# Performance work log

Hardware: AMD Instinct MI355X
Metric: run time of the kernel (lower is better)

Reference implementation:

```python
import jax, jax.numpy as jnp
import numpy as np

B, C, H, W = 8, 128, 48, 48
RED = 16  # SELayer reduction


def setup_inputs() -> dict:
    key = jax.random.key(0)
    ks = jax.random.split(key, 8)
    s = 0.05  # weight scale for numerical stability of softmax
    return {
        "x": jax.random.normal(ks[0], (B, C, H, W), jnp.float32),
        "Wq": jax.random.normal(ks[1], (C, C), jnp.float32) * s,
        "bq": jnp.zeros((C,), jnp.float32),
        "Wk": jax.random.normal(ks[2], (C, C), jnp.float32) * s,
        "bk": jnp.zeros((C,), jnp.float32),
        "Wv": jax.random.normal(ks[3], (C, C), jnp.float32) * s,
        "bv": jnp.zeros((C,), jnp.float32),
        "se_w1": jax.random.normal(ks[4], (C // RED, C), jnp.float32) * s,
        "se_w2": jax.random.normal(ks[5], (C, C // RED), jnp.float32) * s,
        "gamma": jax.random.normal(ks[6], (1,), jnp.float32),
    }


def reference(x, Wq, bq, Wk, bk, Wv, bv, se_w1, se_w2, gamma):
    b, c, h, w = x.shape
    n = h * w
    xf = x.reshape(b, c, n)  # (B, C, N)
    # 1x1 convs == per-pixel linear maps over channels
    q = jnp.einsum('oc,bcn->bon', Wq, xf) + bq[None, :, None]  # (B, C, N)
    k = jnp.einsum('oc,bcn->bon', Wk, xf) + bk[None, :, None]
    v = jnp.einsum('oc,bcn->bon', Wv, xf) + bv[None, :, None]
    # energy[b, i, j] = sum_c q[b, c, i] * k[b, c, j]  (unscaled, as in source)
    energy = jnp.einsum('bci,bcj->bij', q, k)  # (B, N, N)
    attn = jax.nn.softmax(energy, axis=-1)
    # out[b, c, i] = sum_j v[b, c, j] * attn[b, i, j]
    out = jnp.einsum('bcj,bij->bci', v, attn).reshape(b, c, h, w)
    # SELayer applied to the input x
    y = jnp.mean(x, axis=(2, 3))  # (B, C) global average pool
    y = jax.nn.relu(y @ se_w1.T)  # (B, C//RED)
    y = jax.nn.sigmoid(y @ se_w2.T)  # (B, C)
    x_se = x * y[:, :, None, None]
    return gamma[0] * out + x_se
```

## Files before the change

### kernel.cpp

```cpp
#include <hip/hip_runtime.h>

typedef _Float16 half8 __attribute__((ext_vector_type(8)));
typedef _Float16 half4 __attribute__((ext_vector_type(4)));
typedef _Float16 half2v __attribute__((ext_vector_type(2)));
typedef float f32x4 __attribute__((ext_vector_type(4)));

#define BATCH 8
#define CH 128
#define NPIX 2304
#define SPLIT 6
#define JPER (NPIX / SPLIT)
#define NT (JPER / 64)
#define BN (BATCH * NPIX)
#define LOG2E 1.44269504088896f

__device__ __forceinline__ f32x4 mfma32(half8 a, half8 b, f32x4 c) {
    return __builtin_amdgcn_mfma_f32_16x16x32_f16(a, b, c, 0, 0, 0);
}
__device__ __forceinline__ f32x4 mfma16(half4 a, half4 b, f32x4 c) {
    return __builtin_amdgcn_mfma_f32_16x16x16f16(a, b, c, 0, 0, 0);
}

__device__ __forceinline__ void gl_lds16(const _Float16* g, _Float16* l) {
    typedef const __attribute__((address_space(1))) unsigned int gu32;
    typedef __attribute__((address_space(3))) unsigned int lu32;
    __builtin_amdgcn_global_load_lds((gu32*)g, (lu32*)l, 16, 0, 0);
}

__global__ __launch_bounds__(256) void k_prep(
        const float* __restrict__ x, const float* __restrict__ Wq,
        const float* __restrict__ Wk, const float* __restrict__ Wv,
        _Float16* __restrict__ Wh, float* __restrict__ y0) {
    const int bid = blockIdx.x;
    const int t = threadIdx.x;
    if (bid < 1024) {
        const int row = bid;
        const float4* p = (const float4*)(x + (size_t)row * NPIX);
        float s = 0.f;
        for (int tt = t; tt < NPIX / 4; tt += 256) {
            float4 v = p[tt];
            s += v.x + v.y + v.z + v.w;
        }
        for (int m = 1; m < 64; m <<= 1) s += __shfl_xor(s, m);
        __shared__ float ls[4];
        if ((t & 63) == 0) ls[t >> 6] = s;
        __syncthreads();
        if (t == 0) y0[row] = (ls[0] + ls[1] + ls[2] + ls[3]) * (1.0f / (float)NPIX);
    } else {
        int i = (bid - 1024) * 256 + t;
        const float* src = (i < 16384) ? Wq : ((i < 32768) ? Wk : Wv);
        Wh[i] = (_Float16)src[i & 16383];
    }
}

__global__ __launch_bounds__(256) void k_proj(
        const float* __restrict__ x, const _Float16* __restrict__ Wh,
        const float* __restrict__ bq, const float* __restrict__ bk, const float* __restrict__ bv,
        _Float16* __restrict__ qT, _Float16* __restrict__ kT, _Float16* __restrict__ vN,
        const float* __restrict__ y0, const float* __restrict__ se_w1,
        const float* __restrict__ se_w2, float* __restrict__ scale) {
    const int which = blockIdx.z;
    const int t = threadIdx.x;

    if (which == 3) {
        if (blockIdx.x != 0 || blockIdx.y != 0) return;
        __shared__ float ly[128];
        __shared__ float ly1[8];
        for (int b = 0; b < BATCH; ++b) {
            if (t < 128) ly[t] = y0[b * 128 + t];
            __syncthreads();
            if (t < 8) {
                float a = 0.f;
                for (int c = 0; c < 128; ++c) a += se_w1[t * 128 + c] * ly[c];
                ly1[t] = fmaxf(a, 0.f);
            }
            __syncthreads();
            if (t < 128) {
                float a = 0.f;
                for (int r = 0; r < 8; ++r) a += se_w2[t * 8 + r] * ly1[r];
                scale[b * 128 + t] = 1.f / (1.f + __expf(-a));
            }
            __syncthreads();
        }
        return;
    }

    const int n0 = blockIdx.x * 128;
    const int b = blockIdx.y;
    const float* bias = (which == 0) ? bq : ((which == 1) ? bk : bv);
    const _Float16* W = Wh + which * 16384;

    __shared__ __align__(16) _Float16 xt[128 * 128];

    {
        const float* xb = x + (size_t)b * CH * NPIX + n0;
        for (int rep = 0; rep < 8; ++rep) {
            int flat = rep * 256 + t;
            int c2 = (flat >> 5) * 2;
            int n4 = (flat & 31) * 4;
            float4 va = *(const float4*)(xb + (size_t)c2 * NPIX + n4);
            float4 vb = *(const float4*)(xb + (size_t)(c2 + 1) * NPIX + n4);
            int cc = c2 & 7, ck = c2 >> 3;
            *(half2v*)(xt + (n4 + 0) * 128 + ((ck ^ ((n4 + 0) & 7)) * 8) + cc) =
                (half2v){(_Float16)va.x, (_Float16)vb.x};
            *(half2v*)(xt + (n4 + 1) * 128 + ((ck ^ ((n4 + 1) & 7)) * 8) + cc) =
                (half2v){(_Float16)va.y, (_Float16)vb.y};
            *(half2v*)(xt + (n4 + 2) * 128 + ((ck ^ ((n4 + 2) & 7)) * 8) + cc) =
                (half2v){(_Float16)va.z, (_Float16)vb.z};
            *(half2v*)(xt + (n4 + 3) * 128 + ((ck ^ ((n4 + 3) & 7)) * 8) + cc) =
                (half2v){(_Float16)va.w, (_Float16)vb.w};
        }
    }
    __syncthreads();

    const int lane = t & 63, w = t >> 6;
    const int ln15 = lane & 15, quad = lane >> 4;

    f32x4 zero4 = {0.f, 0.f, 0.f, 0.f};
    f32x4 acc[8][2];
    for (int mt = 0; mt < 8; ++mt) { acc[mt][0] = zero4; acc[mt][1] = zero4; }

    for (int ks = 0; ks < 4; ++ks) {
        half8 bf[2];
        for (int nt = 0; nt < 2; ++nt) {
            int row = w * 32 + nt * 16 + ln15;
            int ch = ks * 4 + quad;
            bf[nt] = *(const half8*)(xt + row * 128 + ((ch ^ (row & 7)) * 8));
        }
        for (int mt = 0; mt < 8; ++mt) {
            half8 af = *(const half8*)(W + (mt * 16 + ln15) * 128 + ks * 32 + quad * 8);
            acc[mt][0] = mfma32(af, bf[0], acc[mt][0]);
            acc[mt][1] = mfma32(af, bf[1], acc[mt][1]);
        }
    }
    __syncthreads();

    if (which == 2) {
        for (int mt = 0; mt < 8; ++mt)
            for (int nt = 0; nt < 2; ++nt)
                for (int r = 0; r < 4; ++r) {
                    int c = mt * 16 + quad * 4 + r;
                    int nl = w * 32 + nt * 16 + ln15;
                    xt[c * 128 + (((nl >> 3) ^ (c & 7)) * 8) + (nl & 7)] =
                        (_Float16)(acc[mt][nt][r] + bias[c]);
                }
        __syncthreads();
        _Float16* vb = vN + (size_t)b * CH * NPIX + n0;
        for (int rep = 0; rep < 8; ++rep) {
            int c = rep * 16 + (t >> 4), ch = t & 15;
            *(half8*)(vb + (size_t)c * NPIX + ch * 8) =
                *(const half8*)(xt + c * 128 + ((ch ^ (c & 7)) * 8));
        }
    } else {
        for (int mt = 0; mt < 8; ++mt)
            for (int nt = 0; nt < 2; ++nt)
                for (int r = 0; r < 4; r += 2) {
                    int c = mt * 16 + quad * 4 + r;
                    int nl = w * 32 + nt * 16 + ln15;
                    *(half2v*)(xt + nl * 128 + (((c >> 3) ^ (nl & 7)) * 8) + (c & 7)) =
                        (half2v){(_Float16)(acc[mt][nt][r] + bias[c]),
                                 (_Float16)(acc[mt][nt][r + 1] + bias[c + 1])};
                }
        __syncthreads();
        _Float16* dst = ((which == 0) ? qT : kT) + ((size_t)b * NPIX + n0) * CH;
        for (int rep = 0; rep < 8; ++rep) {
            int nl = rep * 16 + (t >> 4), ch = t & 15;
            *(half8*)(dst + nl * 128 + ch * 8) =
                *(const half8*)(xt + nl * 128 + ((ch ^ (nl & 7)) * 8));
        }
    }
}

__global__ __launch_bounds__(256, 5) void k_attn(
        const _Float16* __restrict__ qT, const _Float16* __restrict__ kT,
        const _Float16* __restrict__ vN,
        _Float16* __restrict__ o_part, float* __restrict__ g_m, float* __restrict__ g_l) {
    const int i0 = blockIdx.x * 64;
    const int b = blockIdx.y;
    const int split = blockIdx.z;
    const int t = threadIdx.x;
    const int lane = t & 63, w = t >> 6;
    const int ln15 = lane & 15, quad = lane >> 4;

    __shared__ __align__(16) _Float16 sh[16384];
    _Float16* k_s = sh;
    _Float16* v_s = sh + 8192;

    half8 qf[4];
    {
        const _Float16* qb = qT + ((size_t)b * NPIX + i0 + w * 16 + ln15) * CH + quad * 8;
        for (int kc = 0; kc < 4; ++kc) qf[kc] = *(const half8*)(qb + kc * 32);
    }

    const _Float16* kbase[4];
    const _Float16* vbase[4];
    #pragma unroll
    for (int r = 0; r < 4; ++r) {
        int idx = r * 4 + w;
        int row = 4 * idx + (lane >> 4);
        int kch = (lane & 15) ^ (row & 7);
        kbase[r] = kT + (size_t)b * NPIX * CH + (size_t)row * CH + kch * 8;
        int c = 8 * idx + (lane >> 3);
        int vch = (lane & 7) ^ (c & 7);
        vbase[r] = vN + (size_t)b * CH * NPIX + (size_t)c * NPIX + vch * 8;
    }

    auto stage = [&](int j0) {
        #pragma unroll
        for (int r = 0; r < 4; ++r)
            gl_lds16(kbase[r] + (size_t)j0 * CH, k_s + (r * 4 + w) * 512);
        #pragma unroll
        for (int r = 0; r < 4; ++r)
            gl_lds16(vbase[r] + j0, v_s + (r * 4 + w) * 512);
    };

    stage(split * JPER);

    f32x4 zero4 = {0.f, 0.f, 0.f, 0.f};
    f32x4 os[8];
    for (int ct = 0; ct < 8; ++ct) os[ct] = zero4;
    float m = -1e30f, l = 0.f;

    for (int it = 0; it < NT; ++it) {
        __syncthreads();

        f32x4 s[4];
        for (int jt = 0; jt < 4; ++jt) s[jt] = zero4;
        __builtin_amdgcn_s_setprio(1);
        for (int jt = 0; jt < 4; ++jt) {
            for (int kc = 0; kc < 4; ++kc) {
                int row = jt * 16 + ln15, ch = kc * 4 + quad;
                half8 kf = *(const half8*)(k_s + row * 128 + ((ch ^ (row & 7)) * 8));
                s[jt] = mfma32(kf, qf[kc], s[jt]);
            }
        }
        __builtin_amdgcn_s_setprio(0);

        float mx = fmaxf(fmaxf(s[0][0], s[0][1]), fmaxf(s[0][2], s[0][3]));
        for (int jt = 1; jt < 4; ++jt)
            mx = fmaxf(mx, fmaxf(fmaxf(s[jt][0], s[jt][1]), fmaxf(s[jt][2], s[jt][3])));
        mx = fmaxf(mx, __shfl_xor(mx, 16));
        mx = fmaxf(mx, __shfl_xor(mx, 32));
        if (!__all(mx - m <= 8.0f)) {
            float mnew = fmaxf(m, mx);
            float alpha = exp2f((m - mnew) * LOG2E);
            for (int ct = 0; ct < 8; ++ct) {
                os[ct][0] *= alpha; os[ct][1] *= alpha;
                os[ct][2] *= alpha; os[ct][3] *= alpha;
            }
            l *= alpha;
            m = mnew;
        }
        float mbias = m * LOG2E;

        float sum = 0.f;
        half4 pf[4];
        for (int jt = 0; jt < 4; ++jt)
            for (int r = 0; r < 4; ++r) {
                float p = exp2f(fmaf(s[jt][r], LOG2E, -mbias));
                sum += p;
                pf[jt][r] = (_Float16)p;
            }
        sum += __shfl_xor(sum, 16);
        sum += __shfl_xor(sum, 32);
        l += sum;

        __builtin_amdgcn_s_setprio(1);
        for (int ct = 0; ct < 8; ++ct) {
            int c = ct * 16 + ln15;
            for (int jt = 0; jt < 4; ++jt) {
                int chunk = jt * 2 + (quad >> 1);
                half4 vf = *(const half4*)(v_s + c * 64 + ((chunk ^ (c & 7)) * 8) + (quad & 1) * 4);
                os[ct] = mfma16(vf, pf[jt], os[ct]);
            }
        }
        __builtin_amdgcn_s_setprio(0);

        if (it < NT - 1) {
            __syncthreads();
            stage(split * JPER + (it + 1) * 64);
        }
    }

    if (quad == 0) {
        int i = i0 + w * 16 + ln15;
        g_m[(size_t)(split * BATCH + b) * NPIX + i] = m;
        g_l[(size_t)(split * BATCH + b) * NPIX + i] = l;
    }
    const float linv = 1.0f / l;
    __syncthreads();
    for (int ct = 0; ct < 8; ++ct)
        for (int r = 0; r < 4; ++r) {
            int c = ct * 16 + quad * 4 + r;
            int il = w * 16 + ln15;
            int chunk = (il >> 3);
            sh[c * 64 + ((chunk ^ (c & 7)) * 8) + (il & 7)] = (_Float16)(os[ct][r] * linv);
        }
    __syncthreads();
    _Float16* op = o_part + (size_t)(split * BATCH + b) * CH * NPIX;
    for (int rep = 0; rep < 4; ++rep) {
        int c = rep * 32 + (t >> 3), ch = t & 7;
        *(half8*)(op + (size_t)c * NPIX + i0 + ch * 8) =
            *(const half8*)(sh + c * 64 + ((ch ^ (c & 7)) * 8));
    }
}

__global__ __launch_bounds__(256) void k_combine(
        const _Float16* __restrict__ o_part, const float* __restrict__ g_m,
        const float* __restrict__ g_l, const float* __restrict__ x,
        const float* __restrict__ scale, const float* __restrict__ gamma_p,
        float* __restrict__ out) {
    const int i0 = blockIdx.x * 64;
    const int b = blockIdx.y;
    const int t = threadIdx.x;
    __shared__ float wl[SPLIT][64];

    if (t < 64) {
        int i = i0 + t;
        float mm[SPLIT], llv[SPLIT];
        float M = -1e30f;
        for (int s = 0; s < SPLIT; ++s) {
            mm[s] = g_m[(size_t)(s * BATCH + b) * NPIX + i];
            llv[s] = g_l[(size_t)(s * BATCH + b) * NPIX + i];
            M = fmaxf(M, mm[s]);
        }
        float L = 0.f, e[SPLIT];
        for (int s = 0; s < SPLIT; ++s) {
            e[s] = exp2f((mm[s] - M) * LOG2E);
            L += e[s] * llv[s];
        }
        float inv = 1.f / L;
        for (int s = 0; s < SPLIT; ++s) wl[s][t] = e[s] * llv[s] * inv;
    }
    __syncthreads();

    const float g = gamma_p[0];
    for (int rep = 0; rep < 4; ++rep) {
        int c = rep * 32 + (t >> 3), i8 = (t & 7) * 8;
        size_t base = ((size_t)b * CH + c) * NPIX + i0 + i8;
        float acc[8] = {0.f, 0.f, 0.f, 0.f, 0.f, 0.f, 0.f, 0.f};
        for (int s = 0; s < SPLIT; ++s) {
            half8 o = *(const half8*)(o_part +
                ((size_t)(s * BATCH + b) * CH + c) * NPIX + i0 + i8);
            for (int e = 0; e < 8; ++e) acc[e] += wl[s][i8 + e] * (float)o[e];
        }
        float sc = scale[b * 128 + c];
        float4 x0 = *(const float4*)(x + base);
        float4 x1 = *(const float4*)(x + base + 4);
        float4 r0, r1;
        r0.x = g * acc[0] + x0.x * sc; r0.y = g * acc[1] + x0.y * sc;
        r0.z = g * acc[2] + x0.z * sc; r0.w = g * acc[3] + x0.w * sc;
        r1.x = g * acc[4] + x1.x * sc; r1.y = g * acc[5] + x1.y * sc;
        r1.z = g * acc[6] + x1.z * sc; r1.w = g * acc[7] + x1.w * sc;
        *(float4*)(out + base) = r0;
        *(float4*)(out + base + 4) = r1;
    }
}

extern "C" void kernel_launch(void* const* d_in, const int* in_sizes, int n_in,
                              void* d_out, int out_size, void* d_ws, size_t ws_size,
                              hipStream_t stream) {
    const float* x     = (const float*)d_in[0];
    const float* Wq    = (const float*)d_in[1];
    const float* bq    = (const float*)d_in[2];
    const float* Wk    = (const float*)d_in[3];
    const float* bk    = (const float*)d_in[4];
    const float* Wv    = (const float*)d_in[5];
    const float* bv    = (const float*)d_in[6];
    const float* se_w1 = (const float*)d_in[7];
    const float* se_w2 = (const float*)d_in[8];
    const float* gamma = (const float*)d_in[9];
    float* out = (float*)d_out;

    char* ws = (char*)d_ws;
    const size_t E = (size_t)BATCH * NPIX * CH;
    _Float16* qT = (_Float16*)(ws);
    _Float16* kT = (_Float16*)(ws + E * 2);
    _Float16* vN = (_Float16*)(ws + E * 4);
    _Float16* op = (_Float16*)(ws + E * 6);
    char* tail   = ws + E * 6 + (size_t)SPLIT * E * 2;
    _Float16* Wh = (_Float16*)(tail);
    float* g_m   = (float*)(tail + 98304);
    float* g_l   = (float*)(tail + 98304 + (size_t)SPLIT * BN * 4);
    float* y0    = (float*)(tail + 98304 + 2 * (size_t)SPLIT * BN * 4);
    float* scale = (float*)(tail + 98304 + 2 * (size_t)SPLIT * BN * 4 + 4096);

    k_prep<<<1216, 256, 0, stream>>>(x, Wq, Wk, Wv, Wh, y0);
    k_proj<<<dim3(NPIX / 128, BATCH, 4), 256, 0, stream>>>(
        x, Wh, bq, bk, bv, qT, kT, vN, y0, se_w1, se_w2, scale);
    k_attn<<<dim3(NPIX / 64, BATCH, SPLIT), 256, 0, stream>>>(
        qT, kT, vN, op, g_m, g_l);
    k_combine<<<dim3(NPIX / 64, BATCH), 256, 0, stream>>>(
        op, g_m, g_l, x, scale, gamma, out);
}
```

Before: 167.8 us.

## Process 128 query rows per attention block to reuse K/V tiles across two halves

Each wave in the attention kernel now handles two 16-row query groups, so every K and V fragment read from LDS feeds two MFMAs. This halves K/V staging traffic per query row. The async global-to-LDS loads are replaced by synchronous register-staged copies with two barriers per tile. The lazy rescale skip and priority hints are dropped, and partial outputs are now stored unnormalised, with the combine step changed to match. The risks are more register pressure (launch bounds drop to 2 blocks per CU), fewer blocks, and loads no longer overlapping compute.

```diff
diff --git a/kernel.cpp b/kernel.cpp
--- a/kernel.cpp
+++ b/kernel.cpp
@@ -19,12 +19,6 @@
 }
 __device__ __forceinline__ f32x4 mfma16(half4 a, half4 b, f32x4 c) {
     return __builtin_amdgcn_mfma_f32_16x16x16f16(a, b, c, 0, 0, 0);
-}
-
-__device__ __forceinline__ void gl_lds16(const _Float16* g, _Float16* l) {
-    typedef const __attribute__((address_space(1))) unsigned int gu32;
-    typedef __attribute__((address_space(3))) unsigned int lu32;
-    __builtin_amdgcn_global_load_lds((gu32*)g, (lu32*)l, 16, 0, 0);
 }
 
 __global__ __launch_bounds__(256) void k_prep(
@@ -171,11 +165,11 @@
     }
 }
 
-__global__ __launch_bounds__(256, 5) void k_attn(
+__global__ __launch_bounds__(256, 2) void k_attn(
         const _Float16* __restrict__ qT, const _Float16* __restrict__ kT,
         const _Float16* __restrict__ vN,
         _Float16* __restrict__ o_part, float* __restrict__ g_m, float* __restrict__ g_l) {
-    const int i0 = blockIdx.x * 64;
+    const int i0 = blockIdx.x * 128;
     const int b = blockIdx.y;
     const int split = blockIdx.z;
     const int t = threadIdx.x;
@@ -186,122 +180,130 @@
     _Float16* k_s = sh;
     _Float16* v_s = sh + 8192;
 
-    half8 qf[4];
-    {
-        const _Float16* qb = qT + ((size_t)b * NPIX + i0 + w * 16 + ln15) * CH + quad * 8;
-        for (int kc = 0; kc < 4; ++kc) qf[kc] = *(const half8*)(qb + kc * 32);
-    }
-
-    const _Float16* kbase[4];
-    const _Float16* vbase[4];
+    half8 qf[2][4];
     #pragma unroll
-    for (int r = 0; r < 4; ++r) {
-        int idx = r * 4 + w;
-        int row = 4 * idx + (lane >> 4);
-        int kch = (lane & 15) ^ (row & 7);
-        kbase[r] = kT + (size_t)b * NPIX * CH + (size_t)row * CH + kch * 8;
-        int c = 8 * idx + (lane >> 3);
-        int vch = (lane & 7) ^ (c & 7);
-        vbase[r] = vN + (size_t)b * CH * NPIX + (size_t)c * NPIX + vch * 8;
-    }
-
-    auto stage = [&](int j0) {
-        #pragma unroll
-        for (int r = 0; r < 4; ++r)
-            gl_lds16(kbase[r] + (size_t)j0 * CH, k_s + (r * 4 + w) * 512);
-        #pragma unroll
-        for (int r = 0; r < 4; ++r)
-            gl_lds16(vbase[r] + j0, v_s + (r * 4 + w) * 512);
-    };
-
-    stage(split * JPER);
+    for (int ih = 0; ih < 2; ++ih) {
+        const _Float16* qb = qT + ((size_t)b * NPIX + i0 + w * 32 + ih * 16 + ln15) * CH + quad * 8;
+        #pragma unroll
+        for (int kc = 0; kc < 4; ++kc) qf[ih][kc] = *(const half8*)(qb + kc * 32);
+    }
 
     f32x4 zero4 = {0.f, 0.f, 0.f, 0.f};
-    f32x4 os[8];
-    for (int ct = 0; ct < 8; ++ct) os[ct] = zero4;
-    float m = -1e30f, l = 0.f;
+    f32x4 os[2][8];
+    #pragma unroll
+    for (int ih = 0; ih < 2; ++ih)
+        for (int ct = 0; ct < 8; ++ct) os[ih][ct] = zero4;
+    float m[2] = {-1e30f, -1e30f}, l[2] = {0.f, 0.f};
 
     for (int it = 0; it < NT; ++it) {
-        __syncthreads();
-
-        f32x4 s[4];
-        for (int jt = 0; jt < 4; ++jt) s[jt] = zero4;
-        __builtin_amdgcn_s_setprio(1);
+        const int j0 = split * JPER + it * 64;
+        __syncthreads();
+        {
+            const _Float16* kb = kT + ((size_t)b * NPIX + j0) * CH;
+            for (int rep = 0; rep < 4; ++rep) {
+                int row = rep * 16 + (t >> 4), ch = t & 15;
+                *(half8*)(k_s + row * 128 + ((ch ^ (row & 7)) * 8)) =
+                    *(const half8*)(kb + row * CH + ch * 8);
+            }
+        }
+        {
+            const _Float16* vb = vN + (size_t)b * CH * NPIX + j0;
+            for (int rep = 0; rep < 4; ++rep) {
+                int c = rep * 32 + (t >> 3), ch = t & 7;
+                *(half8*)(v_s + c * 64 + ((ch ^ (c & 7)) * 8)) =
+                    *(const half8*)(vb + (size_t)c * NPIX + ch * 8);
+            }
+        }
+        __syncthreads();
+
+        f32x4 s[2][4];
+        #pragma unroll
+        for (int jt = 0; jt < 4; ++jt) { s[0][jt] = zero4; s[1][jt] = zero4; }
+        #pragma unroll
         for (int jt = 0; jt < 4; ++jt) {
+            #pragma unroll
             for (int kc = 0; kc < 4; ++kc) {
                 int row = jt * 16 + ln15, ch = kc * 4 + quad;
                 half8 kf = *(const half8*)(k_s + row * 128 + ((ch ^ (row & 7)) * 8));
-                s[jt] = mfma32(kf, qf[kc], s[jt]);
-            }
-        }
-        __builtin_amdgcn_s_setprio(0);
-
-        float mx = fmaxf(fmaxf(s[0][0], s[0][1]), fmaxf(s[0][2], s[0][3]));
-        for (int jt = 1; jt < 4; ++jt)
-            mx = fmaxf(mx, fmaxf(fmaxf(s[jt][0], s[jt][1]), fmaxf(s[jt][2], s[jt][3])));
-        mx = fmaxf(mx, __shfl_xor(mx, 16));
-        mx = fmaxf(mx, __shfl_xor(mx, 32));
-        if (!__all(mx - m <= 8.0f)) {
-            float mnew = fmaxf(m, mx);
-            float alpha = exp2f((m - mnew) * LOG2E);
+                s[0][jt] = mfma32(kf, qf[0][kc], s[0][jt]);
+                s[1][jt] = mfma32(kf, qf[1][kc], s[1][jt]);
+            }
+        }
+
+        half4 pf[2][4];
+        #pragma unroll
+        for (int ih = 0; ih < 2; ++ih) {
+            float mx = fmaxf(fmaxf(s[ih][0][0], s[ih][0][1]), fmaxf(s[ih][0][2], s[ih][0][3]));
+            #pragma unroll
+            for (int jt = 1; jt < 4; ++jt)
+                mx = fmaxf(mx, fmaxf(fmaxf(s[ih][jt][0], s[ih][jt][1]),
+                                     fmaxf(s[ih][jt][2], s[ih][jt][3])));
+            mx = fmaxf(mx, __shfl_xor(mx, 16));
+            mx = fmaxf(mx, __shfl_xor(mx, 32));
+            float mnew = fmaxf(m[ih], mx);
+            float alpha = exp2f((m[ih] - mnew) * LOG2E);
+            m[ih] = mnew;
+            float mbias = mnew * LOG2E;
+
+            float sum = 0.f;
+            #pragma unroll
+            for (int jt = 0; jt < 4; ++jt)
+                #pragma unroll
+                for (int r = 0; r < 4; ++r) {
+                    float p = exp2f(fmaf(s[ih][jt][r], LOG2E, -mbias));
+                    sum += p;
+                    pf[ih][jt][r] = (_Float16)p;
+                }
+            sum += __shfl_xor(sum, 16);
+            sum += __shfl_xor(sum, 32);
+            l[ih] = l[ih] * alpha + sum;
+
+            #pragma unroll
             for (int ct = 0; ct < 8; ++ct) {
-                os[ct][0] *= alpha; os[ct][1] *= alpha;
-                os[ct][2] *= alpha; os[ct][3] *= alpha;
-            }
-            l *= alpha;
-            m = mnew;
-        }
-        float mbias = m * LOG2E;
-
-        float sum = 0.f;
-        half4 pf[4];
-        for (int jt = 0; jt < 4; ++jt)
-            for (int r = 0; r < 4; ++r) {
-                float p = exp2f(fmaf(s[jt][r], LOG2E, -mbias));
-                sum += p;
-                pf[jt][r] = (_Float16)p;
-            }
-        sum += __shfl_xor(sum, 16);
-        sum += __shfl_xor(sum, 32);
-        l += sum;
-
-        __builtin_amdgcn_s_setprio(1);
+                os[ih][ct][0] *= alpha; os[ih][ct][1] *= alpha;
+                os[ih][ct][2] *= alpha; os[ih][ct][3] *= alpha;
+            }
+        }
+
+        #pragma unroll
         for (int ct = 0; ct < 8; ++ct) {
             int c = ct * 16 + ln15;
+            #pragma unroll
             for (int jt = 0; jt < 4; ++jt) {
                 int chunk = jt * 2 + (quad >> 1);
                 half4 vf = *(const half4*)(v_s + c * 64 + ((chunk ^ (c & 7)) * 8) + (quad & 1) * 4);
-                os[ct] = mfma16(vf, pf[jt], os[ct]);
-            }
-        }
-        __builtin_amdgcn_s_setprio(0);
-
-        if (it < NT - 1) {
-            __syncthreads();
-            stage(split * JPER + (it + 1) * 64);
+                os[0][ct] = mfma16(vf, pf[0][jt], os[0][ct]);
+                os[1][ct] = mfma16(vf, pf[1][jt], os[1][ct]);
+            }
         }
     }
 
     if (quad == 0) {
-        int i = i0 + w * 16 + ln15;
-        g_m[(size_t)(split * BATCH + b) * NPIX + i] = m;
-        g_l[(size_t)(split * BATCH + b) * NPIX + i] = l;
-    }
-    const float linv = 1.0f / l;
-    __syncthreads();
-    for (int ct = 0; ct < 8; ++ct)
-        for (int r = 0; r < 4; ++r) {
-            int c = ct * 16 + quad * 4 + r;
-            int il = w * 16 + ln15;
-            int chunk = (il >> 3);
-            sh[c * 64 + ((chunk ^ (c & 7)) * 8) + (il & 7)] = (_Float16)(os[ct][r] * linv);
-        }
+        #pragma unroll
+        for (int ih = 0; ih < 2; ++ih) {
+            int i = i0 + w * 32 + ih * 16 + ln15;
+            g_m[(size_t)(split * BATCH + b) * NPIX + i] = m[ih];
+            g_l[(size_t)(split * BATCH + b) * NPIX + i] = l[ih];
+        }
+    }
+    __syncthreads();
+    #pragma unroll
+    for (int ih = 0; ih < 2; ++ih)
+        #pragma unroll
+        for (int ct = 0; ct < 8; ++ct)
+            #pragma unroll
+            for (int r = 0; r < 4; ++r) {
+                int c = ct * 16 + quad * 4 + r;
+                int il = w * 32 + ih * 16 + ln15;
+                int chunk = il >> 3;
+                sh[c * 128 + ((chunk ^ (c & 7)) * 8) + (il & 7)] = (_Float16)os[ih][ct][r];
+            }
     __syncthreads();
     _Float16* op = o_part + (size_t)(split * BATCH + b) * CH * NPIX;
-    for (int rep = 0; rep < 4; ++rep) {
-        int c = rep * 32 + (t >> 3), ch = t & 7;
+    for (int rep = 0; rep < 8; ++rep) {
+        int c = rep * 16 + (t >> 4), ch = t & 15;
         *(half8*)(op + (size_t)c * NPIX + i0 + ch * 8) =
-            *(const half8*)(sh + c * 64 + ((ch ^ (c & 7)) * 8));
+            *(const half8*)(sh + c * 128 + ((ch ^ (c & 7)) * 8));
     }
 }
 
@@ -330,7 +332,7 @@
             L += e[s] * llv[s];
         }
         float inv = 1.f / L;
-        for (int s = 0; s < SPLIT; ++s) wl[s][t] = e[s] * llv[s] * inv;
+        for (int s = 0; s < SPLIT; ++s) wl[s][t] = e[s] * inv;
     }
     __syncthreads();
 
@@ -388,7 +390,7 @@
     k_prep<<<1216, 256, 0, stream>>>(x, Wq, Wk, Wv, Wh, y0);
     k_proj<<<dim3(NPIX / 128, BATCH, 4), 256, 0, stream>>>(
         x, Wh, bq, bk, bv, qT, kT, vN, y0, se_w1, se_w2, scale);
-    k_attn<<<dim3(NPIX / 64, BATCH, SPLIT), 256, 0, stream>>>(
+    k_attn<<<dim3(NPIX / 128, BATCH, SPLIT), 256, 0, stream>>>(
         qT, kT, vN, op, g_m, g_l);
     k_combine<<<dim3(NPIX / 64, BATCH), 256, 0, stream>>>(
         op, g_m, g_l, x, scale, gamma, out);
```

New measurement: 153.0 us, median of 3. 1.1x faster.
